# Kernel tuning notes

Measured on AMD Instinct MI355X. Metric: run time of the kernel, lower is better.

The kernel has to match this reference:

```python
import jax, jax.numpy as jnp
import numpy as np

N_NODES = 50000
N_EDGES = 800000
IN_CH = 128
OUT_CH = 64
HEADS = 8


def setup_inputs() -> dict:
    key = jax.random.key(0)
    k1, k2, k3, k4 = jax.random.split(key, 4)
    x = jax.random.normal(k1, (N_NODES, IN_CH), dtype=jnp.float32)
    edge_index = jax.random.randint(k2, (2, N_EDGES), 0, N_NODES, dtype=jnp.int32)
    # xavier-uniform-ish scale
    W = jax.random.normal(k3, (IN_CH, OUT_CH), dtype=jnp.float32) * (1.0 / np.sqrt(IN_CH))
    attn_weights = jax.random.normal(k4, (2 * OUT_CH, 1), dtype=jnp.float32) * (1.0 / np.sqrt(2 * OUT_CH))
    return {"x": x, "edge_index": edge_index, "W": W, "attn_weights": attn_weights}


def reference(x, edge_index, W, attn_weights):
    # h: [N, out]
    h = x @ W
    ei, ej = edge_index[0], edge_index[1]
    h_i = h[ei]                      # [E, out] gather by destination
    h_j = h[ej]                      # [E, out] gather by source
    edge_feat = jnp.concatenate([h_i, h_j], axis=-1)  # [E, 2*out]
    logits = jax.nn.leaky_relu(edge_feat @ attn_weights, negative_slope=0.2)  # [E, 1]
    # NOTE: original does softmax over dim=0 -> GLOBAL softmax over all edges
    alpha = jax.nn.softmax(logits, axis=0)  # [E, 1]
    # dropout p=0.6 is a no-op in eval mode (training=False)
    msg = h_j * alpha                # [E, out]
    h_head = jnp.zeros_like(h).at[ei].add(msg)  # scatter-add into destinations
    # All heads share W and attn_weights (see source loop), so with dropout off
    # every head is identical; concat == tile along feature dim.
    return jnp.tile(h_head, (1, HEADS))  # [N, out*heads]
```

## Files before the change

kernel.cpp:

```cpp
#include <hip/hip_runtime.h>

#define N_NODES 50000
#define N_EDGES 800000
#define IN_CH 128
#define OUT_CH 64
#define HEADS 8
#define ROW 512
#define NBLK_G 782
#define NBLK_A 782
#define NBIN 196
#define BINCAP 4608
#define NPARTIAL NBIN
#define MAXDEG 64
#define XS_STRIDE 132
#define WS_STRIDE 136

typedef float f4 __attribute__((ext_vector_type(4)));
typedef short bf16x8 __attribute__((ext_vector_type(8)));

__device__ __forceinline__ float lrelu(float z) {
    return z > 0.0f ? z : 0.2f * z;
}

__device__ __forceinline__ unsigned f2b(float f) {
    unsigned u = __float_as_uint(f);
    return (u + 0x7FFFu + ((u >> 16) & 1u)) >> 16;
}

__global__ __launch_bounds__(256) void gemm_st(const float* __restrict__ x,
                                               const float* __restrict__ W,
                                               const float* __restrict__ attn,
                                               unsigned short* __restrict__ hbuf,
                                               float* __restrict__ s,
                                               float* __restrict__ t,
                                               int* __restrict__ bin_count) {
    __shared__ float xs[64 * XS_STRIDE];
    __shared__ unsigned short wls[64 * WS_STRIDE];
    const int tid = threadIdx.x;
    if (blockIdx.x == 0 && tid < NBIN) bin_count[tid] = 0;
    const int base = blockIdx.x * 64;
    {
        const float4* W4 = (const float4*)W;
#pragma unroll
        for (int j = 0; j < 8; ++j) {
            const int idx = tid + j * 256;
            const int k = idx >> 4;
            const int c = (idx & 15) * 4;
            const float4 v = W4[idx];
            wls[(c + 0) * WS_STRIDE + k] = (unsigned short)f2b(v.x);
            wls[(c + 1) * WS_STRIDE + k] = (unsigned short)f2b(v.y);
            wls[(c + 2) * WS_STRIDE + k] = (unsigned short)f2b(v.z);
            wls[(c + 3) * WS_STRIDE + k] = (unsigned short)f2b(v.w);
        }
    }
    {
        const float4* x4 = (const float4*)x;
#pragma unroll
        for (int j = 0; j < 8; ++j) {
            const int idx = tid + j * 256;
            const int r = idx >> 5;
            const int kq = idx & 31;
            const int row = base + r;
            float4 v = make_float4(0.f, 0.f, 0.f, 0.f);
            if (row < N_NODES) v = x4[row * 32 + kq];
            *(float4*)&xs[r * XS_STRIDE + kq * 4] = v;
        }
    }
    __syncthreads();
    const int w = tid >> 6, lane = tid & 63;
    const int m = lane & 15;
    const int kq = lane >> 4;
    bf16x8 afr[4];
#pragma unroll
    for (int kb = 0; kb < 4; ++kb) {
        const float* p = &xs[(w * 16 + m) * XS_STRIDE + kb * 32 + kq * 8];
        const float4 lo = *(const float4*)p;
        const float4 hi = *(const float4*)(p + 4);
        bf16x8 a;
        a[0] = (short)f2b(lo.x); a[1] = (short)f2b(lo.y);
        a[2] = (short)f2b(lo.z); a[3] = (short)f2b(lo.w);
        a[4] = (short)f2b(hi.x); a[5] = (short)f2b(hi.y);
        a[6] = (short)f2b(hi.z); a[7] = (short)f2b(hi.w);
        afr[kb] = a;
    }
    float sacc[4] = {0.f, 0.f, 0.f, 0.f};
    float tacc[4] = {0.f, 0.f, 0.f, 0.f};
#pragma unroll
    for (int ct = 0; ct < 4; ++ct) {
        f4 acc = {0.f, 0.f, 0.f, 0.f};
#pragma unroll
        for (int kb = 0; kb < 4; ++kb) {
            const bf16x8 b = *(const bf16x8*)&wls[(ct * 16 + m) * WS_STRIDE + kb * 32 + kq * 8];
            acc = __builtin_amdgcn_mfma_f32_16x16x32_bf16(afr[kb], b, acc, 0, 0, 0);
        }
        const float a1 = attn[ct * 16 + m];
        const float a2 = attn[64 + ct * 16 + m];
#pragma unroll
        for (int r = 0; r < 4; ++r) {
            sacc[r] = fmaf(acc[r], a1, sacc[r]);
            tacc[r] = fmaf(acc[r], a2, tacc[r]);
            const int row = base + w * 16 + kq * 4 + r;
            if (row < N_NODES)
                hbuf[row * OUT_CH + ct * 16 + m] = (unsigned short)f2b(acc[r]);
        }
    }
#pragma unroll
    for (int off = 1; off < 16; off <<= 1) {
#pragma unroll
        for (int r = 0; r < 4; ++r) {
            sacc[r] += __shfl_xor(sacc[r], off, 64);
            tacc[r] += __shfl_xor(tacc[r], off, 64);
        }
    }
    if (m == 0) {
#pragma unroll
        for (int r = 0; r < 4; ++r) {
            const int row = base + w * 16 + kq * 4 + r;
            if (row < N_NODES) { s[row] = sacc[r]; t[row] = tacc[r]; }
        }
    }
}

__global__ __launch_bounds__(256) void bin_pass(const int4* __restrict__ ei4,
                                                const int4* __restrict__ ej4,
                                                int* __restrict__ bin_count,
                                                unsigned* __restrict__ binned) {
    __shared__ unsigned hist[NBIN], base_s[NBIN], cur[NBIN];
    const int tid = threadIdx.x;
    if (tid < NBIN) { hist[tid] = 0u; cur[tid] = 0u; }
    __syncthreads();
    const int g = blockIdx.x * 256 + tid;
    const bool act = g < N_EDGES / 4;
    int4 li = make_int4(0, 0, 0, 0), lj = make_int4(0, 0, 0, 0);
    if (act) {
        li = ei4[g];
        lj = ej4[g];
        atomicAdd(&hist[li.x >> 8], 1u);
        atomicAdd(&hist[li.y >> 8], 1u);
        atomicAdd(&hist[li.z >> 8], 1u);
        atomicAdd(&hist[li.w >> 8], 1u);
    }
    __syncthreads();
    if (tid < NBIN) {
        const unsigned c = hist[tid];
        base_s[tid] = c ? (unsigned)atomicAdd(&bin_count[tid], (int)c) : 0u;
    }
    __syncthreads();
    if (act) {
        const unsigned p0 = base_s[li.x >> 8] + atomicAdd(&cur[li.x >> 8], 1u);
        if (p0 < BINCAP) binned[(li.x >> 8) * BINCAP + p0] =
            ((unsigned)(li.x & 255) << 16) | (unsigned)lj.x;
        const unsigned p1 = base_s[li.y >> 8] + atomicAdd(&cur[li.y >> 8], 1u);
        if (p1 < BINCAP) binned[(li.y >> 8) * BINCAP + p1] =
            ((unsigned)(li.y & 255) << 16) | (unsigned)lj.y;
        const unsigned p2 = base_s[li.z >> 8] + atomicAdd(&cur[li.z >> 8], 1u);
        if (p2 < BINCAP) binned[(li.z >> 8) * BINCAP + p2] =
            ((unsigned)(li.z & 255) << 16) | (unsigned)lj.z;
        const unsigned p3 = base_s[li.w >> 8] + atomicAdd(&cur[li.w >> 8], 1u);
        if (p3 < BINCAP) binned[(li.w >> 8) * BINCAP + p3] =
            ((unsigned)(li.w & 255) << 16) | (unsigned)lj.w;
    }
}

__global__ __launch_bounds__(1024) void weight_pass(const unsigned* __restrict__ binned,
                                                    const int* __restrict__ bin_count,
                                                    const float* __restrict__ s,
                                                    const float* __restrict__ t,
                                                    unsigned* __restrict__ cv,
                                                    int* __restrict__ count,
                                                    float* __restrict__ partial) {
    __shared__ unsigned bkt[256 * MAXDEG];
    __shared__ unsigned cnt_l[256];
    __shared__ float s_l[256];
    __shared__ float red[16];
    const int tid = threadIdx.x;
    const int bin = blockIdx.x;
    if (tid < 256) {
        cnt_l[tid] = 0u;
        const int d = bin * 256 + tid;
        s_l[tid] = (d < N_NODES) ? s[d] : 0.0f;
    }
    __syncthreads();
    int n = bin_count[bin];
    if (n > BINCAP) n = BINCAP;
    float zs = 0.0f;
    for (int i = tid; i < n; i += 1024) {
        const unsigned e = binned[bin * BINCAP + i];
        const int dl = (int)((e >> 16) & 255u);
        const int src = (int)(e & 0xFFFFu);
        const float w = __expf(lrelu(s_l[dl] + t[src]));
        zs += w;
        const unsigned r = atomicAdd(&cnt_l[dl], 1u);
        if (r < MAXDEG) bkt[dl * MAXDEG + r] = (f2b(w) << 16) | (unsigned)src;
    }
    __syncthreads();
    {
        uint4* cv4 = (uint4*)(cv + bin * (256 * MAXDEG));
        const uint4* b4 = (const uint4*)bkt;
        for (int i = tid; i < 4096; i += 1024) cv4[i] = b4[i];
    }
    if (tid < 256) {
        const int d = bin * 256 + tid;
        if (d < N_NODES) count[d] = (int)cnt_l[tid];
    }
#pragma unroll
    for (int off = 32; off > 0; off >>= 1)
        zs += __shfl_down(zs, off, 64);
    if ((tid & 63) == 0) red[tid >> 6] = zs;
    __syncthreads();
    if (tid == 0) {
        float v = 0.0f;
#pragma unroll
        for (int k = 0; k < 16; ++k) v += red[k];
        partial[bin] = v;
    }
}

__global__ __launch_bounds__(256) void reduce_Z(const float* __restrict__ partial,
                                                float* __restrict__ invZ) {
    __shared__ float ls[4];
    float v = 0.0f;
    for (int i = threadIdx.x; i < NPARTIAL; i += 256) v += partial[i];
#pragma unroll
    for (int off = 32; off > 0; off >>= 1)
        v += __shfl_down(v, off, 64);
    const int lane = threadIdx.x & 63, w = threadIdx.x >> 6;
    if (lane == 0) ls[w] = v;
    __syncthreads();
    if (threadIdx.x == 0) *invZ = 1.0f / (ls[0] + ls[1] + ls[2] + ls[3]);
}

__global__ __launch_bounds__(256) void gather_out(const int* __restrict__ count,
                                                  const unsigned* __restrict__ cv,
                                                  const float* __restrict__ invZ,
                                                  const unsigned short* __restrict__ hbuf,
                                                  float* __restrict__ out) {
    const int n = blockIdx.x * 4 + (threadIdx.x >> 6);
    const int lane = threadIdx.x & 63;
    const int slot = lane >> 3;
    const int q = lane & 7;
    const float z = invZ[0];
    int cnt = count[n];
    cnt = cnt < MAXDEG ? cnt : MAXDEG;
    const int base = n * MAXDEG;
    const uint4* h4 = (const uint4*)hbuf;
    f4 a0 = (f4)(0.0f);
    f4 a1 = (f4)(0.0f);
    unsigned pk = 0u;
    if (slot < cnt) pk = cv[base + slot];
    for (int i = 0; i < cnt; i += 8) {
        const int c = (int)(pk & 0xFFFFu);
        const float w = __uint_as_float(pk & 0xFFFF0000u);
        unsigned pk_n = 0u;
        const int ee = i + 8 + slot;
        if (ee < cnt) pk_n = cv[base + ee];
        const uint4 hv = h4[c * 8 + q];
        a0.x = fmaf(w, __uint_as_float(hv.x << 16),        a0.x);
        a0.y = fmaf(w, __uint_as_float(hv.x & 0xFFFF0000u), a0.y);
        a0.z = fmaf(w, __uint_as_float(hv.y << 16),        a0.z);
        a0.w = fmaf(w, __uint_as_float(hv.y & 0xFFFF0000u), a0.w);
        a1.x = fmaf(w, __uint_as_float(hv.z << 16),        a1.x);
        a1.y = fmaf(w, __uint_as_float(hv.z & 0xFFFF0000u), a1.y);
        a1.z = fmaf(w, __uint_as_float(hv.w << 16),        a1.z);
        a1.w = fmaf(w, __uint_as_float(hv.w & 0xFFFF0000u), a1.w);
        pk = pk_n;
    }
#pragma unroll
    for (int off = 8; off <= 32; off <<= 1) {
        a0.x += __shfl_xor(a0.x, off, 64);
        a0.y += __shfl_xor(a0.y, off, 64);
        a0.z += __shfl_xor(a0.z, off, 64);
        a0.w += __shfl_xor(a0.w, off, 64);
        a1.x += __shfl_xor(a1.x, off, 64);
        a1.y += __shfl_xor(a1.y, off, 64);
        a1.z += __shfl_xor(a1.z, off, 64);
        a1.w += __shfl_xor(a1.w, off, 64);
    }
    a0 *= z;
    a1 *= z;
    f4* out4 = (f4*)out;
    const int ob = n * 128 + slot * 16 + q * 2;
    __builtin_nontemporal_store(a0, out4 + ob);
    __builtin_nontemporal_store(a1, out4 + ob + 1);
}

extern "C" void kernel_launch(void* const* d_in, const int* in_sizes, int n_in,
                              void* d_out, int out_size, void* d_ws, size_t ws_size,
                              hipStream_t stream) {
    const float* x    = (const float*)d_in[0];
    const int*   eidx = (const int*)d_in[1];
    const float* W    = (const float*)d_in[2];
    const float* attn = (const float*)d_in[3];
    float* out = (float*)d_out;

    unsigned short* hbuf = (unsigned short*)d_ws;
    unsigned* cv    = (unsigned*)(hbuf + N_NODES * OUT_CH);
    float* s        = (float*)(cv + NBIN * 256 * MAXDEG);
    float* t        = s + N_NODES;
    float* partial  = t + N_NODES;
    float* invZ     = partial + NPARTIAL;
    int*   bin_count= (int*)(invZ + 1);
    unsigned* binned= (unsigned*)(bin_count + NBIN);

    const int4* ei4 = (const int4*)eidx;
    const int4* ej4 = (const int4*)(eidx + N_EDGES);
    int* count = (int*)(binned + NBIN * BINCAP);

    gemm_st    <<<NBLK_G, 256, 0, stream>>>(x, W, attn, hbuf, s, t, bin_count);
    bin_pass   <<<NBLK_A, 256, 0, stream>>>(ei4, ej4, bin_count, binned);
    weight_pass<<<NBIN, 1024, 0, stream>>>(binned, bin_count, s, t, cv, count, partial);
    reduce_Z   <<<1, 256, 0, stream>>>(partial, invZ);
    gather_out <<<N_NODES / 4, 256, 0, stream>>>(count, cv, invZ, hbuf, out);
}
```

Before: 192.3 us.

## Fuse GEMM and edge binning into one launch, replace Z reduce with atomic

Merges the GEMM kernel and the edge-binning kernel into a single launch that interleaves blocks: odd blocks bin edges, even blocks do the GEMM, so the two independent phases can run concurrently. The separate reduce_Z kernel is removed; weight_pass now atomically adds its partial sums into a single Z value, and gather_out computes the reciprocal itself. x is converted to bf16 when staged into shared memory, which removes the per-fragment conversion and halves LDS use. A memset replaces the in-kernel zeroing of bin counts, and the atomic float sum makes the result order-dependent.

After: 173.8 us. 9.7% less time.

```diff
diff --git a/kernel.cpp b/kernel.cpp
--- a/kernel.cpp
+++ b/kernel.cpp
@@ -10,9 +10,7 @@
 #define NBLK_A 782
 #define NBIN 196
 #define BINCAP 4608
-#define NPARTIAL NBIN
 #define MAXDEG 64
-#define XS_STRIDE 132
 #define WS_STRIDE 136
 
 typedef float f4 __attribute__((ext_vector_type(4)));
@@ -27,18 +25,62 @@
     return (u + 0x7FFFu + ((u >> 16) & 1u)) >> 16;
 }
 
-__global__ __launch_bounds__(256) void gemm_st(const float* __restrict__ x,
-                                               const float* __restrict__ W,
-                                               const float* __restrict__ attn,
-                                               unsigned short* __restrict__ hbuf,
-                                               float* __restrict__ s,
-                                               float* __restrict__ t,
-                                               int* __restrict__ bin_count) {
-    __shared__ float xs[64 * XS_STRIDE];
+__global__ __launch_bounds__(256) void gemm_bin(const float* __restrict__ x,
+                                                const float* __restrict__ W,
+                                                const float* __restrict__ attn,
+                                                const int4* __restrict__ ei4,
+                                                const int4* __restrict__ ej4,
+                                                unsigned short* __restrict__ hbuf,
+                                                float* __restrict__ s,
+                                                float* __restrict__ t,
+                                                int* __restrict__ bin_count,
+                                                unsigned* __restrict__ binned) {
+    __shared__ unsigned short xs[64 * WS_STRIDE];
     __shared__ unsigned short wls[64 * WS_STRIDE];
     const int tid = threadIdx.x;
-    if (blockIdx.x == 0 && tid < NBIN) bin_count[tid] = 0;
-    const int base = blockIdx.x * 64;
+    const int bid = blockIdx.x;
+
+    if (bid & 1) {
+        unsigned* hist = (unsigned*)xs;
+        unsigned* bse  = hist + NBIN;
+        unsigned* cur  = bse + NBIN;
+        if (tid < NBIN) { hist[tid] = 0u; cur[tid] = 0u; }
+        __syncthreads();
+        const int g = (bid >> 1) * 256 + tid;
+        const bool act = g < N_EDGES / 4;
+        int4 li = make_int4(0, 0, 0, 0), lj = make_int4(0, 0, 0, 0);
+        if (act) {
+            li = ei4[g];
+            lj = ej4[g];
+            atomicAdd(&hist[li.x >> 8], 1u);
+            atomicAdd(&hist[li.y >> 8], 1u);
+            atomicAdd(&hist[li.z >> 8], 1u);
+            atomicAdd(&hist[li.w >> 8], 1u);
+        }
+        __syncthreads();
+        if (tid < NBIN) {
+            const unsigned c = hist[tid];
+            bse[tid] = c ? (unsigned)atomicAdd(&bin_count[tid], (int)c) : 0u;
+        }
+        __syncthreads();
+        if (act) {
+            const unsigned p0 = bse[li.x >> 8] + atomicAdd(&cur[li.x >> 8], 1u);
+            if (p0 < BINCAP) binned[(li.x >> 8) * BINCAP + p0] =
+                ((unsigned)(li.x & 255) << 16) | (unsigned)lj.x;
+            const unsigned p1 = bse[li.y >> 8] + atomicAdd(&cur[li.y >> 8], 1u);
+            if (p1 < BINCAP) binned[(li.y >> 8) * BINCAP + p1] =
+                ((unsigned)(li.y & 255) << 16) | (unsigned)lj.y;
+            const unsigned p2 = bse[li.z >> 8] + atomicAdd(&cur[li.z >> 8], 1u);
+            if (p2 < BINCAP) binned[(li.z >> 8) * BINCAP + p2] =
+                ((unsigned)(li.z & 255) << 16) | (unsigned)lj.z;
+            const unsigned p3 = bse[li.w >> 8] + atomicAdd(&cur[li.w >> 8], 1u);
+            if (p3 < BINCAP) binned[(li.w >> 8) * BINCAP + p3] =
+                ((unsigned)(li.w & 255) << 16) | (unsigned)lj.w;
+        }
+        return;
+    }
+
+    const int base = (bid >> 1) * 64;
     {
         const float4* W4 = (const float4*)W;
 #pragma unroll
@@ -63,7 +105,12 @@
             const int row = base + r;
             float4 v = make_float4(0.f, 0.f, 0.f, 0.f);
             if (row < N_NODES) v = x4[row * 32 + kq];
-            *(float4*)&xs[r * XS_STRIDE + kq * 4] = v;
+            ushort4 pb;
+            pb.x = (unsigned short)f2b(v.x);
+            pb.y = (unsigned short)f2b(v.y);
+            pb.z = (unsigned short)f2b(v.z);
+            pb.w = (unsigned short)f2b(v.w);
+            *(ushort4*)&xs[r * WS_STRIDE + kq * 4] = pb;
         }
     }
     __syncthreads();
@@ -72,17 +119,8 @@
     const int kq = lane >> 4;
     bf16x8 afr[4];
 #pragma unroll
-    for (int kb = 0; kb < 4; ++kb) {
-        const float* p = &xs[(w * 16 + m) * XS_STRIDE + kb * 32 + kq * 8];
-        const float4 lo = *(const float4*)p;
-        const float4 hi = *(const float4*)(p + 4);
-        bf16x8 a;
-        a[0] = (short)f2b(lo.x); a[1] = (short)f2b(lo.y);
-        a[2] = (short)f2b(lo.z); a[3] = (short)f2b(lo.w);
-        a[4] = (short)f2b(hi.x); a[5] = (short)f2b(hi.y);
-        a[6] = (short)f2b(hi.z); a[7] = (short)f2b(hi.w);
-        afr[kb] = a;
-    }
+    for (int kb = 0; kb < 4; ++kb)
+        afr[kb] = *(const bf16x8*)&xs[(w * 16 + m) * WS_STRIDE + kb * 32 + kq * 8];
     float sacc[4] = {0.f, 0.f, 0.f, 0.f};
     float tacc[4] = {0.f, 0.f, 0.f, 0.f};
 #pragma unroll
@@ -121,54 +159,13 @@
     }
 }
 
-__global__ __launch_bounds__(256) void bin_pass(const int4* __restrict__ ei4,
-                                                const int4* __restrict__ ej4,
-                                                int* __restrict__ bin_count,
-                                                unsigned* __restrict__ binned) {
-    __shared__ unsigned hist[NBIN], base_s[NBIN], cur[NBIN];
-    const int tid = threadIdx.x;
-    if (tid < NBIN) { hist[tid] = 0u; cur[tid] = 0u; }
-    __syncthreads();
-    const int g = blockIdx.x * 256 + tid;
-    const bool act = g < N_EDGES / 4;
-    int4 li = make_int4(0, 0, 0, 0), lj = make_int4(0, 0, 0, 0);
-    if (act) {
-        li = ei4[g];
-        lj = ej4[g];
-        atomicAdd(&hist[li.x >> 8], 1u);
-        atomicAdd(&hist[li.y >> 8], 1u);
-        atomicAdd(&hist[li.z >> 8], 1u);
-        atomicAdd(&hist[li.w >> 8], 1u);
-    }
-    __syncthreads();
-    if (tid < NBIN) {
-        const unsigned c = hist[tid];
-        base_s[tid] = c ? (unsigned)atomicAdd(&bin_count[tid], (int)c) : 0u;
-    }
-    __syncthreads();
-    if (act) {
-        const unsigned p0 = base_s[li.x >> 8] + atomicAdd(&cur[li.x >> 8], 1u);
-        if (p0 < BINCAP) binned[(li.x >> 8) * BINCAP + p0] =
-            ((unsigned)(li.x & 255) << 16) | (unsigned)lj.x;
-        const unsigned p1 = base_s[li.y >> 8] + atomicAdd(&cur[li.y >> 8], 1u);
-        if (p1 < BINCAP) binned[(li.y >> 8) * BINCAP + p1] =
-            ((unsigned)(li.y & 255) << 16) | (unsigned)lj.y;
-        const unsigned p2 = base_s[li.z >> 8] + atomicAdd(&cur[li.z >> 8], 1u);
-        if (p2 < BINCAP) binned[(li.z >> 8) * BINCAP + p2] =
-            ((unsigned)(li.z & 255) << 16) | (unsigned)lj.z;
-        const unsigned p3 = base_s[li.w >> 8] + atomicAdd(&cur[li.w >> 8], 1u);
-        if (p3 < BINCAP) binned[(li.w >> 8) * BINCAP + p3] =
-            ((unsigned)(li.w & 255) << 16) | (unsigned)lj.w;
-    }
-}
-
 __global__ __launch_bounds__(1024) void weight_pass(const unsigned* __restrict__ binned,
                                                     const int* __restrict__ bin_count,
                                                     const float* __restrict__ s,
                                                     const float* __restrict__ t,
                                                     unsigned* __restrict__ cv,
                                                     int* __restrict__ count,
-                                                    float* __restrict__ partial) {
+                                                    float* __restrict__ Zsum) {
     __shared__ unsigned bkt[256 * MAXDEG];
     __shared__ unsigned cnt_l[256];
     __shared__ float s_l[256];
@@ -212,34 +209,20 @@
         float v = 0.0f;
 #pragma unroll
         for (int k = 0; k < 16; ++k) v += red[k];
-        partial[bin] = v;
-    }
-}
-
-__global__ __launch_bounds__(256) void reduce_Z(const float* __restrict__ partial,
-                                                float* __restrict__ invZ) {
-    __shared__ float ls[4];
-    float v = 0.0f;
-    for (int i = threadIdx.x; i < NPARTIAL; i += 256) v += partial[i];
-#pragma unroll
-    for (int off = 32; off > 0; off >>= 1)
-        v += __shfl_down(v, off, 64);
-    const int lane = threadIdx.x & 63, w = threadIdx.x >> 6;
-    if (lane == 0) ls[w] = v;
-    __syncthreads();
-    if (threadIdx.x == 0) *invZ = 1.0f / (ls[0] + ls[1] + ls[2] + ls[3]);
+        atomicAdd(Zsum, v);
+    }
 }
 
 __global__ __launch_bounds__(256) void gather_out(const int* __restrict__ count,
                                                   const unsigned* __restrict__ cv,
-                                                  const float* __restrict__ invZ,
+                                                  const float* __restrict__ Zsum,
                                                   const unsigned short* __restrict__ hbuf,
                                                   float* __restrict__ out) {
     const int n = blockIdx.x * 4 + (threadIdx.x >> 6);
     const int lane = threadIdx.x & 63;
     const int slot = lane >> 3;
     const int q = lane & 7;
-    const float z = invZ[0];
+    const float z = 1.0f / Zsum[0];
     int cnt = count[n];
     cnt = cnt < MAXDEG ? cnt : MAXDEG;
     const int base = n * MAXDEG;
@@ -297,18 +280,17 @@
     unsigned* cv    = (unsigned*)(hbuf + N_NODES * OUT_CH);
     float* s        = (float*)(cv + NBIN * 256 * MAXDEG);
     float* t        = s + N_NODES;
-    float* partial  = t + N_NODES;
-    float* invZ     = partial + NPARTIAL;
-    int*   bin_count= (int*)(invZ + 1);
-    unsigned* binned= (unsigned*)(bin_count + NBIN);
+    int* bin_count  = (int*)(t + N_NODES);
+    float* Zsum     = (float*)(bin_count + NBIN);
+    unsigned* binned= (unsigned*)(Zsum + 1);
+    int* count      = (int*)(binned + NBIN * BINCAP);
 
     const int4* ei4 = (const int4*)eidx;
     const int4* ej4 = (const int4*)(eidx + N_EDGES);
-    int* count = (int*)(binned + NBIN * BINCAP);
-
-    gemm_st    <<<NBLK_G, 256, 0, stream>>>(x, W, attn, hbuf, s, t, bin_count);
-    bin_pass   <<<NBLK_A, 256, 0, stream>>>(ei4, ej4, bin_count, binned);
-    weight_pass<<<NBIN, 1024, 0, stream>>>(binned, bin_count, s, t, cv, count, partial);
-    reduce_Z   <<<1, 256, 0, stream>>>(partial, invZ);
-    gather_out <<<N_NODES / 4, 256, 0, stream>>>(count, cv, invZ, hbuf, out);
-}
+
+    hipMemsetAsync(bin_count, 0, (NBIN + 1) * sizeof(int), stream);
+    gemm_bin   <<<NBLK_G + NBLK_A, 256, 0, stream>>>(x, W, attn, ei4, ej4,
+                                                     hbuf, s, t, bin_count, binned);
+    weight_pass<<<NBIN, 1024, 0, stream>>>(binned, bin_count, s, t, cv, count, Zsum);
+    gather_out <<<N_NODES / 4, 256, 0, stream>>>(count, cv, Zsum, hbuf, out);
+}
```
